# Kernel tuning notes

Measured on AMD Instinct MI355X. Metric: run time of the kernel, lower is better.

## Reference

```python
import jax, jax.numpy as jnp
import numpy as np

N_NODES = 100000
N_FEAT = 512
HIDDEN = 16
N_CLASSES = 7
N_EDGES = 3200000


def gcn_conv(x, W, b, src, dst, num_nodes):
    """GCNConv: add self-loops, symmetric deg^-1/2 normalization, linear, aggregate."""
    loop = jnp.arange(num_nodes, dtype=src.dtype)
    src2 = jnp.concatenate([src, loop])  # [E+N]
    dst2 = jnp.concatenate([dst, loop])
    ones = jnp.ones(src2.shape[0], dtype=x.dtype)
    deg = jax.ops.segment_sum(ones, dst2, num_segments=num_nodes)  # in-degree incl. self-loop
    dinv = jnp.where(deg > 0, jax.lax.rsqrt(deg), 0.0)
    norm = dinv[src2] * dinv[dst2]  # [E+N]
    h = x @ W  # [N, out] -- transform before gather (small out dim)
    msg = h[src2] * norm[:, None]  # gather + scale
    out = jax.ops.segment_sum(msg, dst2, num_segments=num_nodes)  # scatter-add
    return out + b


def setup_inputs() -> dict:
    key = jax.random.key(0)
    k1, k2, k3, k4, k5 = jax.random.split(key, 5)
    x = jax.random.normal(k1, (N_NODES, N_FEAT), dtype=jnp.float32)
    edge_index = jax.random.randint(k2, (2, N_EDGES), 0, N_NODES, dtype=jnp.int64)
    # Glorot init like PyG GCNConv
    W1 = jax.random.normal(k3, (N_FEAT, HIDDEN), dtype=jnp.float32) * np.sqrt(2.0 / (N_FEAT + HIDDEN))
    b1 = jnp.zeros((HIDDEN,), dtype=jnp.float32)
    W2 = jax.random.normal(k4, (HIDDEN, N_CLASSES), dtype=jnp.float32) * np.sqrt(2.0 / (HIDDEN + N_CLASSES))
    b2 = jnp.zeros((N_CLASSES,), dtype=jnp.float32)
    return {"x": x, "edge_index": edge_index, "W1": W1, "b1": b1, "W2": W2, "b2": b2}


def reference(x, edge_index, W1, b1, W2, b2):
    src, dst = edge_index[0], edge_index[1]
    h = gcn_conv(x, W1, b1, src, dst, N_NODES)
    h = jax.nn.relu(h)
    # F.dropout(training=self.training): identity in eval mode (deterministic reference)
    h = gcn_conv(h, W2, b2, src, dst, N_NODES)
    return jax.nn.log_softmax(h, axis=1)
```

## Files before the change

kernel.cpp:

```cpp
#include <hip/hip_runtime.h>
#include <math.h>

#define N_NODES   100000
#define N_FEAT    512
#define HIDDEN    16
#define N_CLASSES 7
#define N_EDGES   3200000

#define BSHIFT 7
#define BNODES 128
#define BMASK  127
#define NBUK   782
#define CHUNK  16384
#define NCHUNK 196
#define CAP    6144

typedef short v8s __attribute__((ext_vector_type(8)));
typedef float v4f __attribute__((ext_vector_type(4)));

__device__ __forceinline__ float bf_lo(unsigned int p) { return __uint_as_float(p << 16); }
__device__ __forceinline__ float bf_hi(unsigned int p) { return __uint_as_float(p & 0xffff0000u); }
__device__ __forceinline__ unsigned int pack_bf2(float a, float b) {
    unsigned int ua = __float_as_uint(a); ua += 0x7fffu + ((ua >> 16) & 1u);
    unsigned int ub = __float_as_uint(b); ub += 0x7fffu + ((ub >> 16) & 1u);
    return (ua >> 16) | (ub & 0xffff0000u);
}


__global__ __launch_bounds__(1024) void k_hist(const int* __restrict__ dst,
                                               int* __restrict__ hglob) {
    __shared__ int h[NBUK];
    int tid = threadIdx.x;
    for (int i = tid; i < NBUK; i += 1024) h[i] = 0;
    __syncthreads();
    int base = blockIdx.x * CHUNK;
    for (int i = tid; i < CHUNK; i += 1024) {
        int e = base + i;
        if (e < N_EDGES) atomicAdd(&h[dst[e] >> BSHIFT], 1);
    }
    __syncthreads();
    for (int i = tid; i < NBUK; i += 1024)
        hglob[blockIdx.x * NBUK + i] = h[i];
}


__global__ __launch_bounds__(1024) void k_scan(const int* __restrict__ hglob,
                                               int* __restrict__ btot,
                                               int* __restrict__ gbase,
                                               int* __restrict__ hpre) {
    __shared__ int sd[1024];
    int t = threadIdx.x;
    int tot = 0;
    if (t < NBUK)
        for (int c = 0; c < NCHUNK; c++) tot += hglob[c * NBUK + t];
    sd[t] = (t < NBUK) ? tot : 0;
    __syncthreads();
    for (int off = 1; off < 1024; off <<= 1) {
        int a = (t >= off) ? sd[t - off] : 0;
        __syncthreads();
        sd[t] += a;
        __syncthreads();
    }
    if (t < NBUK) {
        int ex = sd[t] - tot;
        btot[t] = tot;
        gbase[t] = ex;
        int run = ex;
        for (int c = 0; c < NCHUNK; c++) {
            hpre[c * NBUK + t] = run;
            run += hglob[c * NBUK + t];
        }
    }
}


__global__ __launch_bounds__(1024) void k_scatter(const int* __restrict__ src,
                                                  const int* __restrict__ dst,
                                                  const int* __restrict__ hpre,
                                                  int* __restrict__ entries) {
    __shared__ int lb[NBUK];
    __shared__ int cur[NBUK];
    __shared__ int lbase[NBUK];
    __shared__ int sd[1024];
    __shared__ int sbuf[CHUNK];
    __shared__ unsigned short sbk[CHUNK];
    int tid = threadIdx.x;
    int base = blockIdx.x * CHUNK;

    for (int i = tid; i < NBUK; i += 1024) {
        lb[i] = hpre[blockIdx.x * NBUK + i];
        cur[i] = 0;
    }
    __syncthreads();

    int myent[16];
    int mypos[16];
#pragma unroll
    for (int u = 0; u < 16; u++) {
        int e = base + u * 1024 + tid;
        int en = 0, bp = -1;
        if (e < N_EDGES) {
            int d = dst[e];
            int b = d >> BSHIFT;
            int r = atomicAdd(&cur[b], 1);
            en = src[e] | ((d & BMASK) << 17);
            bp = (b << 14) | r;
        }
        myent[u] = en;
        mypos[u] = bp;
    }
    __syncthreads();

    int v = (tid < NBUK) ? cur[tid] : 0;
    sd[tid] = v;
    __syncthreads();
    for (int off = 1; off < 1024; off <<= 1) {
        int a = (tid >= off) ? sd[tid - off] : 0;
        __syncthreads();
        sd[tid] += a;
        __syncthreads();
    }
    if (tid < NBUK) lbase[tid] = sd[tid] - v;
    __syncthreads();

#pragma unroll
    for (int u = 0; u < 16; u++) {
        int bp = mypos[u];
        if (bp >= 0) {
            int b = bp >> 14, r = bp & 0x3FFF;
            int p = lbase[b] + r;
            sbuf[p] = myent[u];
            sbk[p] = (unsigned short)b;
        }
    }
    __syncthreads();

    int lim = N_EDGES - base;
    if (lim > CHUNK) lim = CHUNK;
    for (int i = tid; i < lim; i += 1024) {
        int b = sbk[i];
        entries[lb[b] + (i - lbase[b])] = sbuf[i];
    }
}


__global__ __launch_bounds__(512) void k_nodesort(int* __restrict__ entries,
                                                  const int* __restrict__ btot,
                                                  const int* __restrict__ gbase,
                                                  float* __restrict__ dinv,
                                                  int* __restrict__ nodeptr) {
    __shared__ int ebuf[CAP];
    __shared__ int hcnt[BNODES];
    __shared__ int hincl[BNODES];
    __shared__ int hcur[BNODES];
    int tid = threadIdx.x;
    int bk = blockIdx.x;
    int cnt = btot[bk], base = gbase[bk];
    if (cnt > CAP) cnt = CAP;
    if (tid < BNODES) hcnt[tid] = 0;
    __syncthreads();
    for (int i = tid; i < cnt; i += 512) {
        int en = entries[base + i];
        ebuf[i] = en;
        atomicAdd(&hcnt[en >> 17], 1);
    }
    __syncthreads();
    if (tid < BNODES) hincl[tid] = hcnt[tid];
    __syncthreads();
    for (int off = 1; off < BNODES; off <<= 1) {
        int v = 0;
        if (tid < BNODES && tid >= off) v = hincl[tid - off];
        __syncthreads();
        if (tid < BNODES) hincl[tid] += v;
        __syncthreads();
    }
    if (tid < BNODES) {
        int excl = hincl[tid] - hcnt[tid];
        hcur[tid] = excl;
        int n = bk * BNODES + tid;
        if (n < N_NODES) {
            nodeptr[n] = base + excl;
            dinv[n]    = rsqrtf((float)(hcnt[tid] + 1));
        } else if (n == N_NODES) {
            nodeptr[n] = base + excl;
        }
    }
    __syncthreads();
    for (int i = tid; i < cnt; i += 512) {
        int en = ebuf[i];
        int pos = atomicAdd(&hcur[en >> 17], 1);
        entries[base + pos] = en & 0x1FFFF;
    }
}


__global__ __launch_bounds__(256) void k_gemm1(const float* __restrict__ x,
                                               const float* __restrict__ W1,
                                               const float* __restrict__ dinv,
                                               unsigned int* __restrict__ hs1b) {
    __shared__ unsigned int wfrag[16 * 64 * 4];
    __shared__ unsigned int atile[64 * 68];

    int tid = threadIdx.x;
    int wave = tid >> 6, lane = tid & 63;
    int row0 = blockIdx.x * 64;
    int m = lane & 15, quad = lane >> 4;

    {
        int q0 = tid * 4;
#pragma unroll
        for (int qq = 0; qq < 4; qq++) {
            int q = q0 + qq;
            int s = q >> 6, l = q & 63;
            int n = l & 15, kb = s * 32 + (l >> 4) * 8;
            unsigned int* wp = &wfrag[q * 4];
#pragma unroll
            for (int h = 0; h < 4; h++)
                wp[h] = pack_bf2(W1[(kb + 2 * h) * 16 + n],
                                 W1[(kb + 2 * h + 1) * 16 + n]);
        }
    }

    v4f acc = {0.f, 0.f, 0.f, 0.f};

    for (int c = 0; c < 4; c++) {
        __syncthreads();
#pragma unroll
        for (int i = 0; i < 8; i++) {
            int f = i * 256 + tid;
            int r = f >> 5, c4 = f & 31;
            int grow = row0 + r;
            float4 xv = make_float4(0.f, 0.f, 0.f, 0.f);
            if (grow < N_NODES)
                xv = *(const float4*)(x + (size_t)grow * N_FEAT + c * 128 + c4 * 4);
            unsigned int* ap = &atile[r * 68 + c4 * 2];
            ap[0] = pack_bf2(xv.x, xv.y);
            ap[1] = pack_bf2(xv.z, xv.w);
        }
        __syncthreads();
#pragma unroll
        for (int s = 0; s < 4; s++) {
            v8s af = *(const v8s*)&atile[(wave * 16 + m) * 68 + s * 16 + quad * 4];
            v8s bf = *(const v8s*)&wfrag[((c * 4 + s) * 64 + lane) * 4];
            acc = __builtin_amdgcn_mfma_f32_16x16x32_bf16(af, bf, acc, 0, 0, 0);
        }
    }

    __syncthreads();
    float* dt = (float*)atile;
    {
        float* wdt = dt + wave * 272;
        int col = lane & 15;
#pragma unroll
        for (int r = 0; r < 4; r++)
            wdt[(quad * 4 + r) * 17 + col] = acc[r];
    }
    __syncthreads();
    {
        int row = tid >> 2, p = tid & 3;
        int grow = row0 + row;
        if (grow < N_NODES) {
            float dn = dinv[grow];
            float* wdt = dt + (row >> 4) * 272 + (row & 15) * 17 + 4 * p;
            unsigned int d0 = pack_bf2(dn * wdt[0], dn * wdt[1]);
            unsigned int d1 = pack_bf2(dn * wdt[2], dn * wdt[3]);
            *(uint2*)(hs1b + (size_t)grow * 8 + 2 * p) = make_uint2(d0, d1);
        }
    }
}


__global__ __launch_bounds__(512) void k_agg1(const unsigned int* __restrict__ hs1b,
                                              const int* __restrict__ srt,
                                              const int* __restrict__ nodeptr,
                                              const float* __restrict__ dinv,
                                              const float* __restrict__ b1,
                                              const float* __restrict__ W2,
                                              unsigned int* __restrict__ hs2b) {
    __shared__ float w2l[HIDDEN * N_CLASSES];
    __shared__ float b1l[HIDDEN];
    __shared__ float part[BNODES][17];
    int tid = threadIdx.x;
    if (tid < HIDDEN * N_CLASSES) w2l[tid] = W2[tid];
    if (tid < HIDDEN) b1l[tid] = b1[tid];

    int bk = blockIdx.x;
    int g = tid >> 1, j = tid & 1;
    int l = g & (BNODES - 1), half = g >> 7;
    int n = bk * BNODES + l;
    bool valid = (n < N_NODES);

    float accL[4] = {0.f, 0.f, 0.f, 0.f};
    float accH[4] = {0.f, 0.f, 0.f, 0.f};
    const uint4* hv = (const uint4*)hs1b;

    if (valid) {
        int p0 = nodeptr[n], p1 = nodeptr[n + 1];
        int mid = p0 + ((p1 - p0) >> 1);
        int e0 = half ? mid : p0;
        int e1 = half ? p1 : mid;
        int e = e0;
        for (; e + 4 <= e1; e += 4) {
            int s[4];
            uint4 v[4];
#pragma unroll
            for (int u = 0; u < 4; u++) s[u] = srt[e + u];
#pragma unroll
            for (int u = 0; u < 4; u++) v[u] = hv[(size_t)s[u] * 2 + j];
#pragma unroll
            for (int u = 0; u < 4; u++) {
                accL[0] += bf_lo(v[u].x); accH[0] += bf_hi(v[u].x);
                accL[1] += bf_lo(v[u].y); accH[1] += bf_hi(v[u].y);
                accL[2] += bf_lo(v[u].z); accH[2] += bf_hi(v[u].z);
                accL[3] += bf_lo(v[u].w); accH[3] += bf_hi(v[u].w);
            }
        }
        for (; e < e1; e++) {
            uint4 v0 = hv[(size_t)srt[e] * 2 + j];
            accL[0] += bf_lo(v0.x); accH[0] += bf_hi(v0.x);
            accL[1] += bf_lo(v0.y); accH[1] += bf_hi(v0.y);
            accL[2] += bf_lo(v0.z); accH[2] += bf_hi(v0.z);
            accL[3] += bf_lo(v0.w); accH[3] += bf_hi(v0.w);
        }
        if (half == 0) {
            uint4 sv = hv[(size_t)n * 2 + j];
            accL[0] += bf_lo(sv.x); accH[0] += bf_hi(sv.x);
            accL[1] += bf_lo(sv.y); accH[1] += bf_hi(sv.y);
            accL[2] += bf_lo(sv.z); accH[2] += bf_hi(sv.z);
            accL[3] += bf_lo(sv.w); accH[3] += bf_hi(sv.w);
        }
    }

    if (half == 1 && valid) {
#pragma unroll
        for (int q = 0; q < 4; q++) {
            int ch = j * 8 + 2 * q;
            part[l][ch]     = accL[q];
            part[l][ch + 1] = accH[q];
        }
    }
    __syncthreads();

    if (half == 0 && valid) {
        float dn = dinv[n];
        float t[7] = {0.f, 0.f, 0.f, 0.f, 0.f, 0.f, 0.f};
#pragma unroll
        for (int q = 0; q < 4; q++) {
            int ch = j * 8 + 2 * q;
            float z0 = fmaxf(dn * (accL[q] + part[l][ch])     + b1l[ch],     0.f);
            float z1 = fmaxf(dn * (accH[q] + part[l][ch + 1]) + b1l[ch + 1], 0.f);
            const float* w0 = &w2l[ch * 7];
            const float* w1 = &w2l[(ch + 1) * 7];
#pragma unroll
            for (int k = 0; k < 7; k++) t[k] += z0 * w0[k] + z1 * w1[k];
        }
#pragma unroll
        for (int k = 0; k < 7; k++) t[k] += __shfl_xor(t[k], 1, 64);
        if (j == 0) {
            uint4 o;
            o.x = pack_bf2(dn * t[0], dn * t[1]);
            o.y = pack_bf2(dn * t[2], dn * t[3]);
            o.z = pack_bf2(dn * t[4], dn * t[5]);
            o.w = pack_bf2(dn * t[6], 0.f);
            ((uint4*)hs2b)[n] = o;
        }
    }
}


__global__ __launch_bounds__(512) void k_agg2(const unsigned int* __restrict__ hs2b,
                                              const int* __restrict__ srt,
                                              const int* __restrict__ nodeptr,
                                              const float* __restrict__ dinv,
                                              const float* __restrict__ b2,
                                              float* __restrict__ out) {
    int tid = threadIdx.x;
    int bk = blockIdx.x;
    int l = tid >> 2, h = tid & 3;
    int n = bk * BNODES + l;
    bool valid = (n < N_NODES);

    float a[8] = {0.f, 0.f, 0.f, 0.f, 0.f, 0.f, 0.f, 0.f};
    const uint4* hv = (const uint4*)hs2b;

    if (valid) {
        int p0 = nodeptr[n], p1 = nodeptr[n + 1];
        int deg = p1 - p0;
        int e0 = p0 + ((deg * h) >> 2);
        int e1 = p0 + ((deg * (h + 1)) >> 2);
        int e = e0;
        for (; e + 4 <= e1; e += 4) {
            int s[4];
            uint4 v[4];
#pragma unroll
            for (int u = 0; u < 4; u++) s[u] = srt[e + u];
#pragma unroll
            for (int u = 0; u < 4; u++) v[u] = hv[s[u]];
#pragma unroll
            for (int u = 0; u < 4; u++) {
                a[0] += bf_lo(v[u].x); a[1] += bf_hi(v[u].x);
                a[2] += bf_lo(v[u].y); a[3] += bf_hi(v[u].y);
                a[4] += bf_lo(v[u].z); a[5] += bf_hi(v[u].z);
                a[6] += bf_lo(v[u].w);
            }
        }
        for (; e < e1; e++) {
            uint4 v0 = hv[srt[e]];
            a[0] += bf_lo(v0.x); a[1] += bf_hi(v0.x);
            a[2] += bf_lo(v0.y); a[3] += bf_hi(v0.y);
            a[4] += bf_lo(v0.z); a[5] += bf_hi(v0.z);
            a[6] += bf_lo(v0.w);
        }
        if (h == 0) {
            uint4 sv = hv[n];
            a[0] += bf_lo(sv.x); a[1] += bf_hi(sv.x);
            a[2] += bf_lo(sv.y); a[3] += bf_hi(sv.y);
            a[4] += bf_lo(sv.z); a[5] += bf_hi(sv.z);
            a[6] += bf_lo(sv.w);
        }
#pragma unroll
        for (int q = 0; q < 7; q++) {
            a[q] += __shfl_xor(a[q], 1, 64);
            a[q] += __shfl_xor(a[q], 2, 64);
        }
        if (h == 0) {
            float dn = dinv[n];
            float lg[7];
#pragma unroll
            for (int c = 0; c < 7; c++) lg[c] = dn * a[c] + b2[c];
            float m = lg[0];
#pragma unroll
            for (int c = 1; c < 7; c++) m = fmaxf(m, lg[c]);
            float s = 0.f;
#pragma unroll
            for (int c = 0; c < 7; c++) s += expf(lg[c] - m);
            float ls = m + logf(s);
#pragma unroll
            for (int c = 0; c < 7; c++) out[(size_t)n * 7 + c] = lg[c] - ls;
        }
    }
}


extern "C" void kernel_launch(void* const* d_in, const int* in_sizes, int n_in,
                              void* d_out, int out_size, void* d_ws, size_t ws_size,
                              hipStream_t stream) {
    const float* x  = (const float*)d_in[0];
    const int*   ei = (const int*)d_in[1];
    const float* W1 = (const float*)d_in[2];
    const float* b1 = (const float*)d_in[3];
    const float* W2 = (const float*)d_in[4];
    const float* b2 = (const float*)d_in[5];
    float* out = (float*)d_out;

    const int* src = ei;
    const int* dst = ei + N_EDGES;

    char* w = (char*)d_ws;
    int*          btot    = (int*)(w + 0);
    int*          gbase   = (int*)(w + 4096);
    float*        dinv    = (float*)(w + 8192);
    int*          nodeptr = (int*)(w + 408576);
    int*          hglob   = (int*)(w + 808960);
    int*          hpre    = (int*)(w + 1422336);
    unsigned int* hs1b    = (unsigned int*)(w + 2036736);
    unsigned int* hs2b    = (unsigned int*)(w + 5236736);
    int*          entries = (int*)(w + 6836736);

    k_hist    <<<NCHUNK, 1024, 0, stream>>>(dst, hglob);
    k_scan    <<<1, 1024, 0, stream>>>(hglob, btot, gbase, hpre);
    k_scatter <<<NCHUNK, 1024, 0, stream>>>(src, dst, hpre, entries);
    k_nodesort<<<NBUK, 512, 0, stream>>>(entries, btot, gbase, dinv, nodeptr);
    k_gemm1   <<<1563, 256, 0, stream>>>(x, W1, dinv, hs1b);
    k_agg1    <<<NBUK, 512, 0, stream>>>(hs1b, entries, nodeptr, dinv, b1, W2, hs2b);
    k_agg2    <<<NBUK, 512, 0, stream>>>(hs2b, entries, nodeptr, dinv, b2, out);
}
```

Baseline: 435.2 us.

## Fuse per-bucket node sort into agg1, prepack W1 once, stream x directly

The per-bucket node sort moves into the first aggregation kernel, so entries are sorted in LDS and consumed in the same block. Only a lightweight degree-count kernel runs before the GEMM, to produce dinv. W1 is packed to bf16 MFMA fragments once by a tiny kernel instead of in every GEMM block. The GEMM now loads x rows straight into registers instead of staging them through an LDS tile. The aim is to cut one full entries pass plus redundant weight packing and LDS traffic. In exchange, entries are read twice (degree pass and agg1) and agg1 uses more LDS and has a longer prologue.

After: 442.3 us. About the same (+1.6%).

```diff
diff --git a/kernel.cpp b/kernel.cpp
--- a/kernel.cpp
+++ b/kernel.cpp
@@ -24,6 +24,24 @@
     unsigned int ua = __float_as_uint(a); ua += 0x7fffu + ((ua >> 16) & 1u);
     unsigned int ub = __float_as_uint(b); ub += 0x7fffu + ((ub >> 16) & 1u);
     return (ua >> 16) | (ub & 0xffff0000u);
+}
+
+
+__global__ __launch_bounds__(256) void k_wpack(const float* __restrict__ W1,
+                                               unsigned int* __restrict__ wfrag_g) {
+    int tid = threadIdx.x;
+    int q0 = tid * 4;
+#pragma unroll
+    for (int qq = 0; qq < 4; qq++) {
+        int q = q0 + qq;
+        int s = q >> 6, l = q & 63;
+        int n = l & 15, kb = s * 32 + (l >> 4) * 8;
+        unsigned int* wp = &wfrag_g[q * 4];
+#pragma unroll
+        for (int h = 0; h < 4; h++)
+            wp[h] = pack_bf2(W1[(kb + 2 * h) * 16 + n],
+                             W1[(kb + 2 * h + 1) * 16 + n]);
+    }
 }
 
 
@@ -144,21 +162,113 @@
 }
 
 
-__global__ __launch_bounds__(512) void k_nodesort(int* __restrict__ entries,
-                                                  const int* __restrict__ btot,
-                                                  const int* __restrict__ gbase,
-                                                  float* __restrict__ dinv,
-                                                  int* __restrict__ nodeptr) {
+__global__ __launch_bounds__(256) void k_deg(const int* __restrict__ entries,
+                                             const int* __restrict__ btot,
+                                             const int* __restrict__ gbase,
+                                             float* __restrict__ dinv) {
+    __shared__ int hcnt[BNODES];
+    int tid = threadIdx.x;
+    int bk = blockIdx.x;
+    if (tid < BNODES) hcnt[tid] = 0;
+    __syncthreads();
+    int cnt = btot[bk], base = gbase[bk];
+    for (int i = tid; i < cnt; i += 256)
+        atomicAdd(&hcnt[entries[base + i] >> 17], 1);
+    __syncthreads();
+    if (tid < BNODES) {
+        int n = bk * BNODES + tid;
+        if (n < N_NODES) dinv[n] = rsqrtf((float)(hcnt[tid] + 1));
+    }
+}
+
+
+__global__ __launch_bounds__(256) void k_gemm1(const float* __restrict__ x,
+                                               const unsigned int* __restrict__ wfrag_g,
+                                               const float* __restrict__ dinv,
+                                               unsigned int* __restrict__ hs1b) {
+    __shared__ unsigned int wfrag[16 * 64 * 4];
+    __shared__ float dtile[4 * 16 * 17];
+
+    int tid = threadIdx.x;
+    int wave = tid >> 6, lane = tid & 63;
+    int row0 = blockIdx.x * 64;
+    int m = lane & 15, quad = lane >> 4;
+
+    {
+        const uint4* wg = (const uint4*)wfrag_g;
+        uint4* wl = (uint4*)wfrag;
+        for (int i = tid; i < 1024; i += 256) wl[i] = wg[i];
+    }
+
+    int grow = row0 + wave * 16 + m;
+    bool vrow = (grow < N_NODES);
+    const float* xr = x + (size_t)(vrow ? grow : 0) * N_FEAT + quad * 8;
+
+    v4f acc = {0.f, 0.f, 0.f, 0.f};
+    __syncthreads();
+
+#pragma unroll
+    for (int c = 0; c < 16; c++) {
+        float4 xa = make_float4(0.f, 0.f, 0.f, 0.f);
+        float4 xb = make_float4(0.f, 0.f, 0.f, 0.f);
+        if (vrow) {
+            xa = *(const float4*)(xr + c * 32);
+            xb = *(const float4*)(xr + c * 32 + 4);
+        }
+        unsigned int pa[4] = {pack_bf2(xa.x, xa.y), pack_bf2(xa.z, xa.w),
+                              pack_bf2(xb.x, xb.y), pack_bf2(xb.z, xb.w)};
+        v8s af;
+        __builtin_memcpy(&af, pa, 16);
+        v8s bf = *(const v8s*)&wfrag[(c * 64 + lane) * 4];
+        acc = __builtin_amdgcn_mfma_f32_16x16x32_bf16(af, bf, acc, 0, 0, 0);
+    }
+
+    {
+        float* wdt = dtile + wave * 272;
+#pragma unroll
+        for (int r = 0; r < 4; r++)
+            wdt[(quad * 4 + r) * 17 + m] = acc[r];
+    }
+    __syncthreads();
+    {
+        int row = tid >> 2, p = tid & 3;
+        int orow = row0 + row;
+        if (orow < N_NODES) {
+            float dn = dinv[orow];
+            float* wdt = dtile + (row >> 4) * 272 + (row & 15) * 17 + 4 * p;
+            unsigned int d0 = pack_bf2(dn * wdt[0], dn * wdt[1]);
+            unsigned int d1 = pack_bf2(dn * wdt[2], dn * wdt[3]);
+            *(uint2*)(hs1b + (size_t)orow * 8 + 2 * p) = make_uint2(d0, d1);
+        }
+    }
+}
+
+
+__global__ __launch_bounds__(512) void k_agg1(const unsigned int* __restrict__ hs1b,
+                                              int* __restrict__ entries,
+                                              const int* __restrict__ btot,
+                                              const int* __restrict__ gbase,
+                                              const float* __restrict__ dinv,
+                                              const float* __restrict__ b1,
+                                              const float* __restrict__ W2,
+                                              unsigned int* __restrict__ hs2b,
+                                              int* __restrict__ nodeptr) {
     __shared__ int ebuf[CAP];
     __shared__ int hcnt[BNODES];
     __shared__ int hincl[BNODES];
     __shared__ int hcur[BNODES];
+    __shared__ float w2l[HIDDEN * N_CLASSES];
+    __shared__ float b1l[HIDDEN];
+    __shared__ float part[BNODES][17];
     int tid = threadIdx.x;
     int bk = blockIdx.x;
+    if (tid < HIDDEN * N_CLASSES) w2l[tid] = W2[tid];
+    if (tid < HIDDEN) b1l[tid] = b1[tid];
+    if (tid < BNODES) hcnt[tid] = 0;
     int cnt = btot[bk], base = gbase[bk];
     if (cnt > CAP) cnt = CAP;
-    if (tid < BNODES) hcnt[tid] = 0;
-    __syncthreads();
+    __syncthreads();
+
     for (int i = tid; i < cnt; i += 512) {
         int en = entries[base + i];
         ebuf[i] = en;
@@ -178,12 +288,7 @@
         int excl = hincl[tid] - hcnt[tid];
         hcur[tid] = excl;
         int n = bk * BNODES + tid;
-        if (n < N_NODES) {
-            nodeptr[n] = base + excl;
-            dinv[n]    = rsqrtf((float)(hcnt[tid] + 1));
-        } else if (n == N_NODES) {
-            nodeptr[n] = base + excl;
-        }
+        if (n <= N_NODES) nodeptr[n] = base + excl;
     }
     __syncthreads();
     for (int i = tid; i < cnt; i += 512) {
@@ -191,100 +296,8 @@
         int pos = atomicAdd(&hcur[en >> 17], 1);
         entries[base + pos] = en & 0x1FFFF;
     }
-}
-
-
-__global__ __launch_bounds__(256) void k_gemm1(const float* __restrict__ x,
-                                               const float* __restrict__ W1,
-                                               const float* __restrict__ dinv,
-                                               unsigned int* __restrict__ hs1b) {
-    __shared__ unsigned int wfrag[16 * 64 * 4];
-    __shared__ unsigned int atile[64 * 68];
-
-    int tid = threadIdx.x;
-    int wave = tid >> 6, lane = tid & 63;
-    int row0 = blockIdx.x * 64;
-    int m = lane & 15, quad = lane >> 4;
-
-    {
-        int q0 = tid * 4;
-#pragma unroll
-        for (int qq = 0; qq < 4; qq++) {
-            int q = q0 + qq;
-            int s = q >> 6, l = q & 63;
-            int n = l & 15, kb = s * 32 + (l >> 4) * 8;
-            unsigned int* wp = &wfrag[q * 4];
-#pragma unroll
-            for (int h = 0; h < 4; h++)
-                wp[h] = pack_bf2(W1[(kb + 2 * h) * 16 + n],
-                                 W1[(kb + 2 * h + 1) * 16 + n]);
-        }
-    }
-
-    v4f acc = {0.f, 0.f, 0.f, 0.f};
-
-    for (int c = 0; c < 4; c++) {
-        __syncthreads();
-#pragma unroll
-        for (int i = 0; i < 8; i++) {
-            int f = i * 256 + tid;
-            int r = f >> 5, c4 = f & 31;
-            int grow = row0 + r;
-            float4 xv = make_float4(0.f, 0.f, 0.f, 0.f);
-            if (grow < N_NODES)
-                xv = *(const float4*)(x + (size_t)grow * N_FEAT + c * 128 + c4 * 4);
-            unsigned int* ap = &atile[r * 68 + c4 * 2];
-            ap[0] = pack_bf2(xv.x, xv.y);
-            ap[1] = pack_bf2(xv.z, xv.w);
-        }
-        __syncthreads();
-#pragma unroll
-        for (int s = 0; s < 4; s++) {
-            v8s af = *(const v8s*)&atile[(wave * 16 + m) * 68 + s * 16 + quad * 4];
-            v8s bf = *(const v8s*)&wfrag[((c * 4 + s) * 64 + lane) * 4];
-            acc = __builtin_amdgcn_mfma_f32_16x16x32_bf16(af, bf, acc, 0, 0, 0);
-        }
-    }
-
-    __syncthreads();
-    float* dt = (float*)atile;
-    {
-        float* wdt = dt + wave * 272;
-        int col = lane & 15;
-#pragma unroll
-        for (int r = 0; r < 4; r++)
-            wdt[(quad * 4 + r) * 17 + col] = acc[r];
-    }
-    __syncthreads();
-    {
-        int row = tid >> 2, p = tid & 3;
-        int grow = row0 + row;
-        if (grow < N_NODES) {
-            float dn = dinv[grow];
-            float* wdt = dt + (row >> 4) * 272 + (row & 15) * 17 + 4 * p;
-            unsigned int d0 = pack_bf2(dn * wdt[0], dn * wdt[1]);
-            unsigned int d1 = pack_bf2(dn * wdt[2], dn * wdt[3]);
-            *(uint2*)(hs1b + (size_t)grow * 8 + 2 * p) = make_uint2(d0, d1);
-        }
-    }
-}
-
-
-__global__ __launch_bounds__(512) void k_agg1(const unsigned int* __restrict__ hs1b,
-                                              const int* __restrict__ srt,
-                                              const int* __restrict__ nodeptr,
-                                              const float* __restrict__ dinv,
-                                              const float* __restrict__ b1,
-                                              const float* __restrict__ W2,
-                                              unsigned int* __restrict__ hs2b) {
-    __shared__ float w2l[HIDDEN * N_CLASSES];
-    __shared__ float b1l[HIDDEN];
-    __shared__ float part[BNODES][17];
-    int tid = threadIdx.x;
-    if (tid < HIDDEN * N_CLASSES) w2l[tid] = W2[tid];
-    if (tid < HIDDEN) b1l[tid] = b1[tid];
-
-    int bk = blockIdx.x;
+    __syncthreads();
+
     int g = tid >> 1, j = tid & 1;
     int l = g & (BNODES - 1), half = g >> 7;
     int n = bk * BNODES + l;
@@ -293,9 +306,11 @@
     float accL[4] = {0.f, 0.f, 0.f, 0.f};
     float accH[4] = {0.f, 0.f, 0.f, 0.f};
     const uint4* hv = (const uint4*)hs1b;
+    const int* srt = entries;
 
     if (valid) {
-        int p0 = nodeptr[n], p1 = nodeptr[n + 1];
+        int p0 = base + hincl[l] - hcnt[l];
+        int p1 = base + hincl[l];
         int mid = p0 + ((p1 - p0) >> 1);
         int e0 = half ? mid : p0;
         int e1 = half ? p1 : mid;
@@ -466,12 +481,14 @@
     unsigned int* hs1b    = (unsigned int*)(w + 2036736);
     unsigned int* hs2b    = (unsigned int*)(w + 5236736);
     int*          entries = (int*)(w + 6836736);
-
+    unsigned int* wfrag_g = (unsigned int*)(w + 19636736);
+
+    k_wpack   <<<1, 256, 0, stream>>>(W1, wfrag_g);
     k_hist    <<<NCHUNK, 1024, 0, stream>>>(dst, hglob);
     k_scan    <<<1, 1024, 0, stream>>>(hglob, btot, gbase, hpre);
     k_scatter <<<NCHUNK, 1024, 0, stream>>>(src, dst, hpre, entries);
-    k_nodesort<<<NBUK, 512, 0, stream>>>(entries, btot, gbase, dinv, nodeptr);
-    k_gemm1   <<<1563, 256, 0, stream>>>(x, W1, dinv, hs1b);
-    k_agg1    <<<NBUK, 512, 0, stream>>>(hs1b, entries, nodeptr, dinv, b1, W2, hs2b);
+    k_deg     <<<NBUK, 256, 0, stream>>>(entries, btot, gbase, dinv);
+    k_gemm1   <<<1563, 256, 0, stream>>>(x, wfrag_g, dinv, hs1b);
+    k_agg1    <<<NBUK, 512, 0, stream>>>(hs1b, entries, btot, gbase, dinv, b1, W2, hs2b, nodeptr);
     k_agg2    <<<NBUK, 512, 0, stream>>>(hs2b, entries, nodeptr, dinv, b2, out);
 }
```
